# Kernel optimization log

Hardware: AMD Instinct MI355X
Metric: run time of the kernel (lower is better)

## Reference

```python
import jax, jax.numpy as jnp
import numpy as np

N_NODES = 50000
N_EDGES = 800000
D = 64
L = 2


def setup_inputs() -> dict:
    key = jax.random.key(0)
    ks = jax.random.split(key, 5)
    h = jax.random.normal(ks[0], (N_NODES, D), dtype=jnp.float32)
    Ws = jax.random.normal(ks[1], (L, D, D), dtype=jnp.float32) / np.sqrt(D)
    bs = jnp.zeros((L, D), dtype=jnp.float32)
    edge_weight = jax.random.uniform(ks[2], (N_EDGES,), dtype=jnp.float32)
    src = jax.random.randint(ks[3], (N_EDGES,), 0, N_NODES, dtype=jnp.int64)
    dst = jax.random.randint(ks[4], (N_EDGES,), 0, N_NODES, dtype=jnp.int64)
    return {"h": h, "Ws": Ws, "bs": bs, "edge_weight": edge_weight, "src": src, "dst": dst}


def reference(h, Ws, bs, edge_weight, src, dst):
    # DGL GraphConv(norm='none', activation=relu) with in_feats==out_feats:
    # aggregate-then-transform: agg[v] = sum_{e:(u->v)} w_e * h[u]; h' = relu(agg @ W + b)
    n = h.shape[0]
    for l in range(Ws.shape[0]):
        msg = h[src] * edge_weight[:, None]                      # [E, D] gather + scale
        agg = jax.ops.segment_sum(msg, dst, num_segments=n)      # [N, D] scatter-add
        h = jax.nn.relu(agg @ Ws[l] + bs[l])
    return h
```

## Files before the change

### kernel.cpp

```cpp
#include <hip/hip_runtime.h>
#include <hip/hip_fp16.h>

#define NN 50000
#define NE 800000
#define DD 64
#define BS 100
#define NB 500
#define ECAP 2048
#define CHUNK 3200
#define NPB 250
#define EPT (ECAP / 256)
#define NGRID (NN / 16)

typedef __attribute__((ext_vector_type(8))) short short8;
typedef __attribute__((ext_vector_type(4))) float f32x4;


__device__ __forceinline__ unsigned packh2(float lo, float hi) {
    __half2 h = __floats2half2_rn(lo, hi);
    return *reinterpret_cast<unsigned*>(&h);
}

__global__ __launch_bounds__(256) void f32_to_f16_zero_kernel(
        const float4* __restrict__ in4, uint4* __restrict__ out4,
        int* __restrict__ gpos, const float* __restrict__ Ws,
        uint4* __restrict__ wfrag) {
    if (blockIdx.x == 0) {
        for (int j = threadIdx.x; j < NB; j += 256) gpos[j] = 0;
    }
    if (blockIdx.x == 1 || blockIdx.x == 2) {
        int L = blockIdx.x - 1;
        const float* W = Ws + L * DD * DD;
        for (int e = threadIdx.x; e < 512; e += 256) {
            int w = e >> 7;
            int s = (e >> 6) & 1;
            int l = e & 63;
            int col = w * 16 + (l & 15);
            int k0 = 32 * s + 8 * (l >> 4);
            uint4 u;
            unsigned* up = (unsigned*)&u;
            #pragma unroll
            for (int uu = 0; uu < 4; ++uu) {
                float lo = W[(k0 + 2 * uu) * DD + col];
                float hi = W[(k0 + 2 * uu + 1) * DD + col];
                up[uu] = packh2(lo, hi);
            }
            wfrag[L * 512 + e] = u;
        }
    }
    int i = blockIdx.x * blockDim.x + threadIdx.x;
    if (i >= NN * DD / 8) return;
    float4 a = in4[2 * i], b = in4[2 * i + 1];
    uint4 o;
    o.x = packh2(a.x, a.y); o.y = packh2(a.z, a.w);
    o.z = packh2(b.x, b.y); o.w = packh2(b.z, b.w);
    out4[i] = o;
}

__global__ __launch_bounds__(1024) void partition_kernel(
        const int* __restrict__ src, const int* __restrict__ dst,
        const float* __restrict__ ew,
        int* __restrict__ gpos, uint2* __restrict__ ebuf) {
    __shared__ int hist[NB];
    __shared__ int base[NB];
    int t = threadIdx.x;
    int c0 = blockIdx.x * CHUNK;

    for (int j = t; j < NB; j += 1024) hist[j] = 0;
    __syncthreads();

    short rank[4];
    int   dcache[4];
    #pragma unroll
    for (int i = 0; i < 4; ++i) {
        int o = i * 1024 + t;
        if (o < CHUNK) {
            int d = dst[c0 + o];
            dcache[i] = d;
            rank[i] = (short)atomicAdd(&hist[d / BS], 1);
        }
    }
    __syncthreads();

    for (int j = t; j < NB; j += 1024) {
        int c = hist[j];
        base[j] = c ? atomicAdd(&gpos[j], c) : 0;
    }
    __syncthreads();

    #pragma unroll
    for (int i = 0; i < 4; ++i) {
        int o = i * 1024 + t;
        if (o < CHUNK) {
            int e = c0 + o;
            int d = dcache[i];
            int bkt = d / BS;
            int dl = d - bkt * BS;
            int pos = base[bkt] + (int)rank[i];
            if (pos < ECAP) {
                ebuf[(size_t)bkt * ECAP + pos] =
                    make_uint2((unsigned)src[e] | ((unsigned)dl << 16),
                               __float_as_uint(ew[e]));
            }
        }
    }
}

__global__ __launch_bounds__(256) void bucket_sort_kernel(
        const uint2* __restrict__ ebuf, const int* __restrict__ gpos,
        unsigned* __restrict__ sorted, int4* __restrict__ nodespan) {
    __shared__ int hist[BS];
    __shared__ int sc[BS];
    __shared__ int dh[128];
    __shared__ int dsc[128];
    int t = threadIdx.x;
    int b = blockIdx.x;
    int cnt = min(gpos[b], ECAP);
    const uint2* slab = ebuf + (size_t)b * ECAP;

    if (t < BS) hist[t] = 0;
    if (t < 128) dh[t] = 0;
    __syncthreads();

    unsigned pay[EPT];
    int dl[EPT], rk[EPT];
    #pragma unroll
    for (int i = 0; i < EPT; ++i) {
        int o = i * 256 + t;
        if (o < cnt) {
            uint2 q = slab[o];
            dl[i]  = (int)(q.x >> 16);
            unsigned w16 = (unsigned)__half_as_ushort(
                __float2half(__uint_as_float(q.y)));
            pay[i] = (q.x & 0xFFFFu) | (w16 << 16);
            rk[i]  = atomicAdd(&hist[dl[i]], 1);
        }
    }
    __syncthreads();

    if (t < BS) sc[t] = hist[t];
    __syncthreads();
    #pragma unroll
    for (int off = 1; off < BS; off <<= 1) {
        int v = (t < BS && t >= off) ? sc[t - off] : 0;
        __syncthreads();
        if (t < BS) sc[t] += v;
        __syncthreads();
    }

    unsigned* oslab = sorted + (size_t)b * ECAP;
    #pragma unroll
    for (int i = 0; i < EPT; ++i) {
        int o = i * 256 + t;
        if (o < cnt) oslab[sc[dl[i]] - hist[dl[i]] + rk[i]] = pay[i];
    }

    if (t < BS) atomicAdd(&dh[min(hist[t], 127)], 1);
    __syncthreads();
    if (t < 128) dsc[t] = dh[t];
    __syncthreads();
    #pragma unroll
    for (int off = 1; off < 128; off <<= 1) {
        int v = (t < 128 && t >= off) ? dsc[t - off] : 0;
        __syncthreads();
        if (t < 128) dsc[t] += v;
        __syncthreads();
    }
    if (t < 128) dh[t] = dsc[t] - dh[t];
    __syncthreads();
    if (t < BS) {
        int d = min(hist[t], 127);
        int p = atomicAdd(&dh[d], 1);
        nodespan[b * BS + p] =
            make_int4(b * ECAP + sc[t] - hist[t], hist[t], b * BS + t, 0);
    }
}

template<bool WRITE_F16>
__global__ __launch_bounds__(256) void gcn_layer_kernel(
        const uint2* __restrict__ hh,
        const unsigned* __restrict__ sorted,
        const int4* __restrict__ nodespan,
        const uint4* __restrict__ wfrag,
        const float* __restrict__ bvec,
        void* __restrict__ outp) {
    __shared__ unsigned Ahf[16 * 36];
    __shared__ float Dls[16 * 68];
    __shared__ int nid[16];
    int t = threadIdx.x;
    int g = t >> 4;
    int lane = t & 15;
    int v = blockIdx.x * 16 + g;

    int4 sp = nodespan[v];
    if (lane == 0) nid[g] = sp.z;
    const unsigned* row = sorted + sp.x;
    int deg = sp.y;

    __half2 z = __floats2half2_rn(0.f, 0.f);
    __half2 a0 = z, a1 = z, b0 = z, b1 = z, c0 = z, c1 = z, d0 = z, d1 = z;
    unsigned ul = (unsigned)lane;
    for (int k0 = 0; k0 < deg; k0 += 16) {
        int kk = k0 + lane;
        unsigned q = (kk < deg) ? row[kk] : 0u;
        int lim = min(16, deg - k0);
        int j = 0;
        for (; j + 4 <= lim; j += 4) {
            unsigned q0 = (unsigned)__shfl((int)q, j + 0, 16);
            unsigned q1 = (unsigned)__shfl((int)q, j + 1, 16);
            unsigned q2 = (unsigned)__shfl((int)q, j + 2, 16);
            unsigned q3 = (unsigned)__shfl((int)q, j + 3, 16);
            uint2 r0 = hh[(q0 & 0xFFFFu) * 16u + ul];
            uint2 r1 = hh[(q1 & 0xFFFFu) * 16u + ul];
            uint2 r2 = hh[(q2 & 0xFFFFu) * 16u + ul];
            uint2 r3 = hh[(q3 & 0xFFFFu) * 16u + ul];
            __half2 w0 = __half2half2(__ushort_as_half((unsigned short)(q0 >> 16)));
            __half2 w1 = __half2half2(__ushort_as_half((unsigned short)(q1 >> 16)));
            __half2 w2 = __half2half2(__ushort_as_half((unsigned short)(q2 >> 16)));
            __half2 w3 = __half2half2(__ushort_as_half((unsigned short)(q3 >> 16)));
            a0 = __hfma2(w0, *(const __half2*)&r0.x, a0);
            a1 = __hfma2(w0, *(const __half2*)&r0.y, a1);
            b0 = __hfma2(w1, *(const __half2*)&r1.x, b0);
            b1 = __hfma2(w1, *(const __half2*)&r1.y, b1);
            c0 = __hfma2(w2, *(const __half2*)&r2.x, c0);
            c1 = __hfma2(w2, *(const __half2*)&r2.y, c1);
            d0 = __hfma2(w3, *(const __half2*)&r3.x, d0);
            d1 = __hfma2(w3, *(const __half2*)&r3.y, d1);
        }
        for (; j < lim; ++j) {
            unsigned q0 = (unsigned)__shfl((int)q, j, 16);
            uint2 r0 = hh[(q0 & 0xFFFFu) * 16u + ul];
            __half2 w0 = __half2half2(__ushort_as_half((unsigned short)(q0 >> 16)));
            a0 = __hfma2(w0, *(const __half2*)&r0.x, a0);
            a1 = __hfma2(w0, *(const __half2*)&r0.y, a1);
        }
    }
    a0 = __hadd2(__hadd2(a0, b0), __hadd2(c0, d0));
    a1 = __hadd2(__hadd2(a1, b1), __hadd2(c1, d1));

    Ahf[g * 36 + 2 * lane]     = *reinterpret_cast<unsigned*>(&a0);
    Ahf[g * 36 + 2 * lane + 1] = *reinterpret_cast<unsigned*>(&a1);
    __syncthreads();

    {
        int w = t >> 6;
        int l = t & 63;
        const uint4* arow = (const uint4*)(&Ahf[(l & 15) * 36]);
        uint4 au0 = arow[l >> 4];
        uint4 au1 = arow[4 + (l >> 4)];
        uint4 bu0 = wfrag[(w * 2 + 0) * 64 + l];
        uint4 bu1 = wfrag[(w * 2 + 1) * 64 + l];
        f32x4 d = {0.f, 0.f, 0.f, 0.f};
        d = __builtin_amdgcn_mfma_f32_16x16x32_f16(
                *(const short8*)&au0, *(const short8*)&bu0, d, 0, 0, 0);
        d = __builtin_amdgcn_mfma_f32_16x16x32_f16(
                *(const short8*)&au1, *(const short8*)&bu1, d, 0, 0, 0);
        #pragma unroll
        for (int r = 0; r < 4; ++r)
            Dls[((l >> 4) * 4 + r) * 68 + w * 16 + (l & 15)] = d[r];
    }
    __syncthreads();

    float4 bias = reinterpret_cast<const float4*>(bvec)[lane];
    float4 dv = *reinterpret_cast<const float4*>(&Dls[g * 68 + lane * 4]);
    float4 o;
    o.x = fmaxf(dv.x + bias.x, 0.f);
    o.y = fmaxf(dv.y + bias.y, 0.f);
    o.z = fmaxf(dv.z + bias.z, 0.f);
    o.w = fmaxf(dv.w + bias.w, 0.f);
    int node = nid[g];
    if (WRITE_F16) {
        reinterpret_cast<uint2*>(outp)[(size_t)node * 16 + lane] =
            make_uint2(packh2(o.x, o.y), packh2(o.z, o.w));
    } else {
        reinterpret_cast<float4*>(outp)[(size_t)node * 16 + lane] = o;
    }
}

extern "C" void kernel_launch(void* const* d_in, const int* in_sizes, int n_in,
                              void* d_out, int out_size, void* d_ws, size_t ws_size,
                              hipStream_t stream) {
    const float* h   = (const float*)d_in[0];
    const float* Ws  = (const float*)d_in[1];
    const float* bs  = (const float*)d_in[2];
    const float* ew  = (const float*)d_in[3];
    const int*   src = (const int*)d_in[4];
    const int*   dst = (const int*)d_in[5];
    float* out = (float*)d_out;
    char* ws = (char*)d_ws;

    int*      gpos     = (int*)(ws);
    uint2*    ebuf     = (uint2*)(ws + 64 * 1024);
    void*     h1       = (void*)(ws + 1u * 1024 * 1024);
    unsigned* sorted   = (unsigned*)(ws + 9u * 1024 * 1024);
    uint4*    wfrag    = (uint4*)(ws + 13u * 1024 * 1024);
    int4*     nodespan = (int4*)(ws + 13u * 1024 * 1024 + 256 * 1024);
    uint2*    h_hf     = (uint2*)(ws + 14u * 1024 * 1024 + 512 * 1024);

    dim3 blk(256);

    f32_to_f16_zero_kernel<<<(NN * DD / 8 + 255) / 256, blk, 0, stream>>>(
        (const float4*)h, (uint4*)h_hf, gpos, Ws, wfrag);
    partition_kernel<<<NPB, dim3(1024), 0, stream>>>(src, dst, ew, gpos, ebuf);
    bucket_sort_kernel<<<NB, blk, 0, stream>>>(ebuf, gpos, sorted, nodespan);

    gcn_layer_kernel<true><<<NGRID, blk, 0, stream>>>(
        h_hf, sorted, nodespan, wfrag, bs, h1);
    gcn_layer_kernel<false><<<NGRID, blk, 0, stream>>>(
        (const uint2*)h1, sorted, nodespan, wfrag + 512, bs + DD, (void*)out);
}
```

Baseline: 64.72 us.

## Fuse bucket sort with layer-0 aggregation and transform using LDS-resident edge lists

Merges the per-bucket sort kernel with the first GCN layer, so each 512-thread block sorts its bucket's edges into LDS and immediately gathers neighbours, runs the MFMA transform and writes the f16 hidden state. This removes one kernel launch and the global re-read of sorted edges and node spans for layer 0. Buckets shrink to 64 nodes (782 buckets, capacity 1280), which lets shifts and masks replace division. The cost is a larger LDS footprint, fewer threads doing the gather per node, and a bucket-capacity limit that silently drops edges if a bucket overflows.

```diff
diff --git a/kernel.cpp b/kernel.cpp
--- a/kernel.cpp
+++ b/kernel.cpp
@@ -4,17 +4,15 @@
 #define NN 50000
 #define NE 800000
 #define DD 64
-#define BS 100
-#define NB 500
-#define ECAP 2048
+#define BS 64
+#define NB 782
+#define ECAP 1280
 #define CHUNK 3200
 #define NPB 250
-#define EPT (ECAP / 256)
-#define NGRID (NN / 16)
+#define NITEMS (NN * DD / 8)
 
 typedef __attribute__((ext_vector_type(8))) short short8;
 typedef __attribute__((ext_vector_type(4))) float f32x4;
-
 
 __device__ __forceinline__ unsigned packh2(float lo, float hi) {
     __half2 h = __floats2half2_rn(lo, hi);
@@ -32,24 +30,20 @@
         int L = blockIdx.x - 1;
         const float* W = Ws + L * DD * DD;
         for (int e = threadIdx.x; e < 512; e += 256) {
-            int w = e >> 7;
-            int s = (e >> 6) & 1;
-            int l = e & 63;
+            int w = e >> 7, s = (e >> 6) & 1, l = e & 63;
             int col = w * 16 + (l & 15);
             int k0 = 32 * s + 8 * (l >> 4);
             uint4 u;
             unsigned* up = (unsigned*)&u;
             #pragma unroll
-            for (int uu = 0; uu < 4; ++uu) {
-                float lo = W[(k0 + 2 * uu) * DD + col];
-                float hi = W[(k0 + 2 * uu + 1) * DD + col];
-                up[uu] = packh2(lo, hi);
-            }
+            for (int uu = 0; uu < 4; ++uu)
+                up[uu] = packh2(W[(k0 + 2 * uu) * DD + col],
+                                W[(k0 + 2 * uu + 1) * DD + col]);
             wfrag[L * 512 + e] = u;
         }
     }
     int i = blockIdx.x * blockDim.x + threadIdx.x;
-    if (i >= NN * DD / 8) return;
+    if (i >= NITEMS) return;
     float4 a = in4[2 * i], b = in4[2 * i + 1];
     uint4 o;
     o.x = packh2(a.x, a.y); o.y = packh2(a.z, a.w);
@@ -65,37 +59,33 @@
     __shared__ int base[NB];
     int t = threadIdx.x;
     int c0 = blockIdx.x * CHUNK;
-
     for (int j = t; j < NB; j += 1024) hist[j] = 0;
     __syncthreads();
-
     short rank[4];
-    int   dcache[4];
+    int dcache[4];
     #pragma unroll
     for (int i = 0; i < 4; ++i) {
         int o = i * 1024 + t;
         if (o < CHUNK) {
             int d = dst[c0 + o];
             dcache[i] = d;
-            rank[i] = (short)atomicAdd(&hist[d / BS], 1);
-        }
-    }
-    __syncthreads();
-
+            rank[i] = (short)atomicAdd(&hist[d >> 6], 1);
+        }
+    }
+    __syncthreads();
     for (int j = t; j < NB; j += 1024) {
         int c = hist[j];
         base[j] = c ? atomicAdd(&gpos[j], c) : 0;
     }
     __syncthreads();
-
     #pragma unroll
     for (int i = 0; i < 4; ++i) {
         int o = i * 1024 + t;
         if (o < CHUNK) {
             int e = c0 + o;
             int d = dcache[i];
-            int bkt = d / BS;
-            int dl = d - bkt * BS;
+            int bkt = d >> 6;
+            int dl = d & 63;
             int pos = base[bkt] + (int)rank[i];
             if (pos < ECAP) {
                 ebuf[(size_t)bkt * ECAP + pos] =
@@ -106,13 +96,19 @@
     }
 }
 
-__global__ __launch_bounds__(256) void bucket_sort_kernel(
+__global__ __launch_bounds__(512, 6) void sort_layer0_kernel(
         const uint2* __restrict__ ebuf, const int* __restrict__ gpos,
-        unsigned* __restrict__ sorted, int4* __restrict__ nodespan) {
-    __shared__ int hist[BS];
-    __shared__ int sc[BS];
-    __shared__ int dh[128];
-    __shared__ int dsc[128];
+        const uint2* __restrict__ hh,
+        const uint4* __restrict__ wfrag,
+        const float* __restrict__ bvec,
+        unsigned* __restrict__ sorted, int4* __restrict__ nodespan,
+        void* __restrict__ h1out) {
+    __shared__ unsigned led[ECAP];
+    __shared__ int hist[BS], sc[BS];
+    __shared__ int dh[128], dsc[128];
+    __shared__ int4 nsp[BS];
+    __shared__ unsigned Ahf[BS * 36];
+    __shared__ float Dls[BS * 68];
     int t = threadIdx.x;
     int b = blockIdx.x;
     int cnt = min(gpos[b], ECAP);
@@ -122,22 +118,21 @@
     if (t < 128) dh[t] = 0;
     __syncthreads();
 
-    unsigned pay[EPT];
-    int dl[EPT], rk[EPT];
-    #pragma unroll
-    for (int i = 0; i < EPT; ++i) {
-        int o = i * 256 + t;
+    unsigned pay[3];
+    int dl[3], rk[3];
+    #pragma unroll
+    for (int i = 0; i < 3; ++i) {
+        int o = i * 512 + t;
         if (o < cnt) {
             uint2 q = slab[o];
-            dl[i]  = (int)(q.x >> 16);
+            dl[i] = (int)(q.x >> 16);
             unsigned w16 = (unsigned)__half_as_ushort(
                 __float2half(__uint_as_float(q.y)));
             pay[i] = (q.x & 0xFFFFu) | (w16 << 16);
-            rk[i]  = atomicAdd(&hist[dl[i]], 1);
-        }
-    }
-    __syncthreads();
-
+            rk[i] = atomicAdd(&hist[dl[i]], 1);
+        }
+    }
+    __syncthreads();
     if (t < BS) sc[t] = hist[t];
     __syncthreads();
     #pragma unroll
@@ -147,15 +142,18 @@
         if (t < BS) sc[t] += v;
         __syncthreads();
     }
-
     unsigned* oslab = sorted + (size_t)b * ECAP;
     #pragma unroll
-    for (int i = 0; i < EPT; ++i) {
-        int o = i * 256 + t;
-        if (o < cnt) oslab[sc[dl[i]] - hist[dl[i]] + rk[i]] = pay[i];
-    }
-
-    if (t < BS) atomicAdd(&dh[min(hist[t], 127)], 1);
+    for (int i = 0; i < 3; ++i) {
+        int o = i * 512 + t;
+        if (o < cnt) {
+            int pos = sc[dl[i]] - hist[dl[i]] + rk[i];
+            led[pos] = pay[i];
+            oslab[pos] = pay[i];
+        }
+    }
+    int nn_b = min(BS, NN - b * BS);
+    if (t < nn_b) atomicAdd(&dh[min(hist[t], 127)], 1);
     __syncthreads();
     if (t < 128) dsc[t] = dh[t];
     __syncthreads();
@@ -168,22 +166,113 @@
     }
     if (t < 128) dh[t] = dsc[t] - dh[t];
     __syncthreads();
-    if (t < BS) {
+    if (t < nn_b) {
         int d = min(hist[t], 127);
         int p = atomicAdd(&dh[d], 1);
+        nsp[p] = make_int4(sc[t] - hist[t], hist[t], b * BS + t, 0);
         nodespan[b * BS + p] =
             make_int4(b * ECAP + sc[t] - hist[t], hist[t], b * BS + t, 0);
-    }
-}
-
-template<bool WRITE_F16>
-__global__ __launch_bounds__(256) void gcn_layer_kernel(
+    } else if (t < BS) {
+        nsp[t] = make_int4(0, 0, NN, 0);
+        nodespan[b * BS + t] = make_int4(0, 0, NN, 0);
+    }
+    __syncthreads();
+
+    int lane = t & 15;
+    unsigned ul = (unsigned)lane;
+    __half2 z = __floats2half2_rn(0.f, 0.f);
+    #pragma unroll
+    for (int pass = 0; pass < 2; ++pass) {
+        int g = (t >> 4) + pass * 32;
+        int4 sp = nsp[g];
+        const unsigned* lrow = led + sp.x;
+        int deg = sp.y;
+        __half2 a0 = z, a1 = z, b0 = z, b1 = z, c0 = z, c1 = z, d0 = z, d1 = z;
+        int j = 0;
+        for (; j + 4 <= deg; j += 4) {
+            unsigned q0 = lrow[j + 0], q1 = lrow[j + 1];
+            unsigned q2 = lrow[j + 2], q3 = lrow[j + 3];
+            uint2 r0 = hh[(q0 & 0xFFFFu) * 16u + ul];
+            uint2 r1 = hh[(q1 & 0xFFFFu) * 16u + ul];
+            uint2 r2 = hh[(q2 & 0xFFFFu) * 16u + ul];
+            uint2 r3 = hh[(q3 & 0xFFFFu) * 16u + ul];
+            __half2 w0 = __half2half2(__ushort_as_half((unsigned short)(q0 >> 16)));
+            __half2 w1 = __half2half2(__ushort_as_half((unsigned short)(q1 >> 16)));
+            __half2 w2 = __half2half2(__ushort_as_half((unsigned short)(q2 >> 16)));
+            __half2 w3 = __half2half2(__ushort_as_half((unsigned short)(q3 >> 16)));
+            a0 = __hfma2(w0, *(const __half2*)&r0.x, a0);
+            a1 = __hfma2(w0, *(const __half2*)&r0.y, a1);
+            b0 = __hfma2(w1, *(const __half2*)&r1.x, b0);
+            b1 = __hfma2(w1, *(const __half2*)&r1.y, b1);
+            c0 = __hfma2(w2, *(const __half2*)&r2.x, c0);
+            c1 = __hfma2(w2, *(const __half2*)&r2.y, c1);
+            d0 = __hfma2(w3, *(const __half2*)&r3.x, d0);
+            d1 = __hfma2(w3, *(const __half2*)&r3.y, d1);
+        }
+        for (; j < deg; ++j) {
+            unsigned q0 = lrow[j];
+            uint2 r0 = hh[(q0 & 0xFFFFu) * 16u + ul];
+            __half2 w0 = __half2half2(__ushort_as_half((unsigned short)(q0 >> 16)));
+            a0 = __hfma2(w0, *(const __half2*)&r0.x, a0);
+            a1 = __hfma2(w0, *(const __half2*)&r0.y, a1);
+        }
+        a0 = __hadd2(__hadd2(a0, b0), __hadd2(c0, d0));
+        a1 = __hadd2(__hadd2(a1, b1), __hadd2(c1, d1));
+        Ahf[g * 36 + 2 * lane]     = *reinterpret_cast<unsigned*>(&a0);
+        Ahf[g * 36 + 2 * lane + 1] = *reinterpret_cast<unsigned*>(&a1);
+    }
+    __syncthreads();
+
+    {
+        int w = t >> 6;
+        int l = t & 63;
+        #pragma unroll
+        for (int i = 0; i < 2; ++i) {
+            int T = w + 8 * i;
+            int rt = T >> 2, ct = T & 3;
+            const uint4* arow = (const uint4*)&Ahf[(rt * 16 + (l & 15)) * 36];
+            uint4 au0 = arow[l >> 4];
+            uint4 au1 = arow[4 + (l >> 4)];
+            uint4 bu0 = wfrag[(ct * 2 + 0) * 64 + l];
+            uint4 bu1 = wfrag[(ct * 2 + 1) * 64 + l];
+            f32x4 d = {0.f, 0.f, 0.f, 0.f};
+            d = __builtin_amdgcn_mfma_f32_16x16x32_f16(
+                    *(const short8*)&au0, *(const short8*)&bu0, d, 0, 0, 0);
+            d = __builtin_amdgcn_mfma_f32_16x16x32_f16(
+                    *(const short8*)&au1, *(const short8*)&bu1, d, 0, 0, 0);
+            #pragma unroll
+            for (int r = 0; r < 4; ++r)
+                Dls[(rt * 16 + (l >> 4) * 4 + r) * 68 + ct * 16 + (l & 15)] = d[r];
+        }
+    }
+    __syncthreads();
+
+    #pragma unroll
+    for (int i = 0; i < 2; ++i) {
+        int idx = i * 512 + t;
+        int g2 = idx >> 4, ln = idx & 15;
+        float4 bias = reinterpret_cast<const float4*>(bvec)[ln];
+        float4 dv = *reinterpret_cast<const float4*>(&Dls[g2 * 68 + ln * 4]);
+        float4 o;
+        o.x = fmaxf(dv.x + bias.x, 0.f);
+        o.y = fmaxf(dv.y + bias.y, 0.f);
+        o.z = fmaxf(dv.z + bias.z, 0.f);
+        o.w = fmaxf(dv.w + bias.w, 0.f);
+        int node = nsp[g2].z;
+        if (node < NN) {
+            reinterpret_cast<uint2*>(h1out)[(size_t)node * 16 + ln] =
+                make_uint2(packh2(o.x, o.y), packh2(o.z, o.w));
+        }
+    }
+}
+
+__global__ __launch_bounds__(256) void gcn_layer1_kernel(
         const uint2* __restrict__ hh,
         const unsigned* __restrict__ sorted,
         const int4* __restrict__ nodespan,
         const uint4* __restrict__ wfrag,
         const float* __restrict__ bvec,
-        void* __restrict__ outp) {
+        float4* __restrict__ outp) {
     __shared__ unsigned Ahf[16 * 36];
     __shared__ float Dls[16 * 68];
     __shared__ int nid[16];
@@ -237,7 +326,6 @@
     }
     a0 = __hadd2(__hadd2(a0, b0), __hadd2(c0, d0));
     a1 = __hadd2(__hadd2(a1, b1), __hadd2(c1, d1));
-
     Ahf[g * 36 + 2 * lane]     = *reinterpret_cast<unsigned*>(&a0);
     Ahf[g * 36 + 2 * lane + 1] = *reinterpret_cast<unsigned*>(&a1);
     __syncthreads();
@@ -269,43 +357,34 @@
     o.z = fmaxf(dv.z + bias.z, 0.f);
     o.w = fmaxf(dv.w + bias.w, 0.f);
     int node = nid[g];
-    if (WRITE_F16) {
-        reinterpret_cast<uint2*>(outp)[(size_t)node * 16 + lane] =
-            make_uint2(packh2(o.x, o.y), packh2(o.z, o.w));
-    } else {
-        reinterpret_cast<float4*>(outp)[(size_t)node * 16 + lane] = o;
-    }
+    if (node < NN) outp[(size_t)node * 16 + lane] = o;
 }
 
 extern "C" void kernel_launch(void* const* d_in, const int* in_sizes, int n_in,
                               void* d_out, int out_size, void* d_ws, size_t ws_size,
                               hipStream_t stream) {
-    const float* h   = (const float*)d_in[0];
-    const float* Ws  = (const float*)d_in[1];
-    const float* bs  = (const float*)d_in[2];
-    const float* ew  = (const float*)d_in[3];
-    const int*   src = (const int*)d_in[4];
-    const int*   dst = (const int*)d_in[5];
-    float* out = (float*)d_out;
+    const float4* h4  = (const float4*)d_in[0];
+    const float*  Ws  = (const float*)d_in[1];
+    const float*  bsv = (const float*)d_in[2];
+    const float*  ew  = (const float*)d_in[3];
+    const int*    src = (const int*)d_in[4];
+    const int*    dst = (const int*)d_in[5];
+    float4* out = (float4*)d_out;
     char* ws = (char*)d_ws;
 
     int*      gpos     = (int*)(ws);
     uint2*    ebuf     = (uint2*)(ws + 64 * 1024);
-    void*     h1       = (void*)(ws + 1u * 1024 * 1024);
     unsigned* sorted   = (unsigned*)(ws + 9u * 1024 * 1024);
     uint4*    wfrag    = (uint4*)(ws + 13u * 1024 * 1024);
     int4*     nodespan = (int4*)(ws + 13u * 1024 * 1024 + 256 * 1024);
     uint2*    h_hf     = (uint2*)(ws + 14u * 1024 * 1024 + 512 * 1024);
-
-    dim3 blk(256);
-
-    f32_to_f16_zero_kernel<<<(NN * DD / 8 + 255) / 256, blk, 0, stream>>>(
-        (const float4*)h, (uint4*)h_hf, gpos, Ws, wfrag);
-    partition_kernel<<<NPB, dim3(1024), 0, stream>>>(src, dst, ew, gpos, ebuf);
-    bucket_sort_kernel<<<NB, blk, 0, stream>>>(ebuf, gpos, sorted, nodespan);
-
-    gcn_layer_kernel<true><<<NGRID, blk, 0, stream>>>(
-        h_hf, sorted, nodespan, wfrag, bs, h1);
-    gcn_layer_kernel<false><<<NGRID, blk, 0, stream>>>(
-        (const uint2*)h1, sorted, nodespan, wfrag + 512, bs + DD, (void*)out);
-}
+    void*     h1       = (void*)(ws + 24u * 1024 * 1024);
+
+    f32_to_f16_zero_kernel<<<(NITEMS + 255) / 256, 256, 0, stream>>>(
+        h4, (uint4*)h_hf, gpos, Ws, wfrag);
+    partition_kernel<<<NPB, 1024, 0, stream>>>(src, dst, ew, gpos, ebuf);
+    sort_layer0_kernel<<<NB, 512, 0, stream>>>(
+        ebuf, gpos, h_hf, wfrag, bsv, sorted, nodespan, h1);
+    gcn_layer1_kernel<<<NN / 16, 256, 0, stream>>>(
+        (const uint2*)h1, sorted, nodespan, wfrag + 512, bsv + DD, out);
+}
```

Measured after the change: 60.55 us. 6.4% less time.
